# Kernel tuning notes

Measured on AMD Instinct MI355X. Metric: run time of the kernel, lower is better.

Reference implementation:

```python
import jax, jax.numpy as jnp
import numpy as np

# Problem constants (from init_kwargs)
NUM_NODES = 120000
NUM_MOVABLE = 100000
NUM_NETS = 100000
NUM_PINS = 400000
NBX = 256
NBY = 256
XL, XH, YL, YH = 0.0, 1000.0, 0.0, 1000.0
BSX = (XH - XL) / NBX  # bin_size_x
BSY = (YH - YL) / NBY  # bin_size_y
UNIT_H_CAP = 1.5  # unit_horizontal_routing_capacity
UNIT_V_CAP = 1.5  # unit_vertical_routing_capacity
MAX_RATE = 2.0    # max_route_opt_adjust_rate
MIN_RATE = 1.0 / MAX_RATE
EPS = 1e-6


def setup_inputs() -> dict:
    key = jax.random.key(0)
    k1, k2, k3, k4, k5, k6, k7, k8 = jax.random.split(key, 8)
    pos = jnp.concatenate([
        jax.random.uniform(k1, (NUM_NODES,), jnp.float32, XL, XH - 10.0),
        jax.random.uniform(k2, (NUM_NODES,), jnp.float32, YL, YH - 10.0)])
    pin_pos = jnp.concatenate([
        jax.random.uniform(k3, (NUM_PINS,), jnp.float32, XL, XH),
        jax.random.uniform(k4, (NUM_PINS,), jnp.float32, YL, YH)])
    node_size_x = jax.random.uniform(k5, (NUM_NODES,), jnp.float32, 1.0, 8.0)
    node_size_y = jax.random.uniform(k6, (NUM_NODES,), jnp.float32, 1.0, 4.0)
    flat_netpin = jax.random.randint(k7, (NUM_PINS,), 0, NUM_PINS, jnp.int32)
    inner = jnp.sort(jax.random.randint(k8, (NUM_NETS - 1,), 0, NUM_PINS, jnp.int32))
    netpin_start = jnp.concatenate([
        jnp.zeros((1,), jnp.int32), inner, jnp.full((1,), NUM_PINS, jnp.int32)])
    return dict(pos=pos, pin_pos=pin_pos, node_size_x=node_size_x,
                node_size_y=node_size_y, netpin_start=netpin_start,
                flat_netpin=flat_netpin)


def _bin_overlap(lo, hi, origin, bin_size, nbins):
    # lo, hi: [K] interval per item; returns [K, nbins] overlap length with each bin
    edges = origin + jnp.arange(nbins, dtype=lo.dtype) * bin_size  # [nbins]
    return jnp.clip(jnp.minimum(hi[:, None], edges + bin_size)
                    - jnp.maximum(lo[:, None], edges), 0.0)


def reference(pos, pin_pos, node_size_x, node_size_y, netpin_start, flat_netpin):
    num_pins = flat_netpin.shape[0]
    # --- per-net bounding boxes from ragged netpin lists (CSR) ---
    slot = jnp.arange(num_pins, dtype=jnp.int32)
    net_id = jnp.clip(jnp.searchsorted(netpin_start, slot, side='right') - 1,
                      0, NUM_NETS - 1)
    px = pin_pos[flat_netpin]
    py = pin_pos[num_pins + flat_netpin]
    xmin = jax.ops.segment_min(px, net_id, NUM_NETS, indices_are_sorted=True)
    xmax = jax.ops.segment_max(px, net_id, NUM_NETS, indices_are_sorted=True)
    ymin = jax.ops.segment_min(py, net_id, NUM_NETS, indices_are_sorted=True)
    ymax = jax.ops.segment_max(py, net_id, NUM_NETS, indices_are_sorted=True)
    valid = (xmax >= xmin) & (ymax >= ymin)  # nets with >=1 pin
    span_x = jnp.where(valid, xmax - xmin, 0.0)
    span_y = jnp.where(valid, ymax - ymin, 0.0)
    # RUDY demand density: horizontal demand per unit area = 1/span_y, etc.
    coef_h = jnp.where(valid & (span_y > EPS), 1.0 / jnp.maximum(span_y, EPS), 0.0)
    coef_v = jnp.where(valid & (span_x > EPS), 1.0 / jnp.maximum(span_x, EPS), 0.0)
    xmin_c = jnp.where(valid, xmin, XL)
    xmax_c = jnp.where(valid, xmax, XL)
    ymin_c = jnp.where(valid, ymin, YL)
    ymax_c = jnp.where(valid, ymax, YL)
    # separable bin overlaps: [N, NBX], [N, NBY]
    ox = _bin_overlap(xmin_c, xmax_c, XL, BSX, NBX)
    oy = _bin_overlap(ymin_c, ymax_c, YL, BSY, NBY)
    # scatter demand into 2D bin grid (rank-1 per net, summed via einsum)
    H = jnp.einsum('nx,ny->xy', ox * coef_h[:, None], oy)
    V = jnp.einsum('nx,ny->xy', ox * coef_v[:, None], oy)
    # capacity adjustment + clamp
    bin_area = BSX * BSY
    util = jnp.maximum(H / (bin_area * UNIT_H_CAP), V / (bin_area * UNIT_V_CAP))
    util = jnp.clip(util, MIN_RATE, MAX_RATE)
    # --- gather bin utilization back per movable node ---
    nxl = pos[:NUM_MOVABLE]
    nyl = pos[NUM_NODES:NUM_NODES + NUM_MOVABLE]
    nxh = nxl + node_size_x[:NUM_MOVABLE]
    nyh = nyl + node_size_y[:NUM_MOVABLE]
    nox = _bin_overlap(nxl, nxh, XL, BSX, NBX)  # [M, NBX]
    noy = _bin_overlap(nyl, nyh, YL, BSY, NBY)  # [M, NBY]
    instance_route_area = jnp.einsum('mx,xy,my->m', nox, util, noy)
    return instance_route_area
```

## Files before the change

### kernel.cpp

```cpp
#include <hip/hip_runtime.h>

#define NUM_NODES   120000
#define NUM_MOVABLE 100000
#define NUM_NETS    100000
#define NUM_PINS    400000
#define NBX 256
#define NBY 256
#define GRID (NBX*NBY)

constexpr float BSX      = 1000.0f / 256.0f;
constexpr float INV_BS   = 256.0f / 1000.0f;
constexpr float BIN_AREA = BSX * BSX;
constexpr float EPSV     = 1e-6f;


__global__ void init_bbox(float4* __restrict__ bbox) {
    int n = blockIdx.x * 256 + threadIdx.x;
    if (n < NUM_NETS) {
        float inf = __uint_as_float(0x7F800000u);
        bbox[n] = make_float4(inf, inf, 0.0f, 0.0f);
    }
}

__global__ void pin_bbox(const float* __restrict__ pin_pos,
                         const int* __restrict__ netpin_start,
                         const int* __restrict__ flat_netpin,
                         float4* __restrict__ bbox) {
    int t = blockIdx.x * 256 + threadIdx.x;
    int key = -4;
    int net = -1, segend = -1;
    float xmn = 3.4e38f, xmx = -3.4e38f, ymn = 3.4e38f, ymx = -3.4e38f;
    if (t < NUM_PINS) {
        int lo = 0, hi = NUM_NETS + 1;
        while (lo < hi) {
            int mid = (lo + hi) >> 1;
            if (netpin_start[mid] <= t) lo = mid + 1; else hi = mid;
        }
        net = min(lo - 1, NUM_NETS - 1);
        int s = netpin_start[net];
        segend = netpin_start[net + 1];
        key = (net << 1) | (s == t ? 1 : 0);
        int p = flat_netpin[t];
        float px = pin_pos[p];
        float py = pin_pos[NUM_PINS + p];
        xmn = px; xmx = px; ymn = py; ymx = py;
    }
    int lane = threadIdx.x & 63;
    for (int d = 1; d < 64; d <<= 1) {
        int   ku = __shfl_up(key, d);
        float a  = __shfl_up(xmn, d);
        float b  = __shfl_up(xmx, d);
        float c  = __shfl_up(ymn, d);
        float e  = __shfl_up(ymx, d);
        if (lane >= d && (ku >> 1) == (key >> 1)) {
            xmn = fminf(xmn, a); xmx = fmaxf(xmx, b);
            ymn = fminf(ymn, c); ymx = fmaxf(ymx, e);
            key |= (ku & 1);
        }
    }
    int nextkey = __shfl_down(key, 1);
    if (t >= NUM_PINS || net < 0) return;
    bool netchg = (lane == 63) ? false : ((nextkey >> 1) != (key >> 1));
    bool tail   = (lane == 63) || netchg;
    if (!tail) return;
    bool true_end  = netchg || (segend == t + 1);
    bool contained = (key & 1) != 0;
    if (contained && true_end) {
        bbox[net] = make_float4(xmn, ymn, xmx, ymx);
    } else {
        unsigned* b = (unsigned*)(bbox + net);
        atomicMin(b + 0, __float_as_uint(xmn));
        atomicMin(b + 1, __float_as_uint(ymn));
        atomicMax(b + 2, __float_as_uint(xmx));
        atomicMax(b + 3, __float_as_uint(ymx));
    }
}

__global__ __launch_bounds__(1024) void splat_rows(
        const float4* __restrict__ bbox,
        float* __restrict__ A_h, float* __restrict__ B_h,
        float* __restrict__ A_v, float* __restrict__ B_v) {
    int bx = blockIdx.x;
    int t  = threadIdx.x;
    __shared__ float F[8][NBY];
    for (int i = t; i < 8 * NBY; i += 1024) ((float*)F)[i] = 0.0f;
    __syncthreads();

    for (int n = t; n < NUM_NETS; n += 1024) {
        float4 b = bbox[n];
        float span_x = b.z - b.x, span_y = b.w - b.y;
        float coef_h = (span_y > EPSV) ? 1.0f / span_y : 0.0f;
        float coef_v = (span_x > EPSV) ? 1.0f / span_x : 0.0f;
        if (coef_h == 0.0f && coef_v == 0.0f) continue;
        int bxl = min((int)(b.x * INV_BS), NBX - 1);
        int bxh = min((int)(b.z * INV_BS), NBX - 1);
        if (bxl != bx && bxh != bx) continue;
        int byl = min((int)(b.y * INV_BS), NBY - 1);
        int byh = min((int)(b.w * INV_BS), NBY - 1);
        float ryl = (float)(byl + 1) * BSX - b.y;
        float ryh = (float)(byh + 1) * BSX - b.w;
        #pragma unroll
        for (int side = 0; side < 2; ++side) {
            bool active = (side == 0) ? (bxl == bx) : (bxh == bx);
            if (!active) continue;
            float rx = (side == 0) ? ((float)(bxl + 1) * BSX - b.x)
                                   : ((float)(bxh + 1) * BSX - b.z);
            float s0 = (side == 0) ? 1.0f : -1.0f;
            if (coef_h != 0.0f) {
                float w0 = s0 * coef_h, w1 = -s0 * coef_h;
                atomicAdd(&F[0][byl], w0 * rx  * ryl);
                atomicAdd(&F[1][byl], w0 * rx  * BSX);
                atomicAdd(&F[2][byl], w0 * BSX * ryl);
                atomicAdd(&F[3][byl], w0 * BSX * BSX);
                atomicAdd(&F[0][byh], w1 * rx  * ryh);
                atomicAdd(&F[1][byh], w1 * rx  * BSX);
                atomicAdd(&F[2][byh], w1 * BSX * ryh);
                atomicAdd(&F[3][byh], w1 * BSX * BSX);
            }
            if (coef_v != 0.0f) {
                float w0 = s0 * coef_v, w1 = -s0 * coef_v;
                atomicAdd(&F[4][byl], w0 * rx  * ryl);
                atomicAdd(&F[5][byl], w0 * rx  * BSX);
                atomicAdd(&F[6][byl], w0 * BSX * ryl);
                atomicAdd(&F[7][byl], w0 * BSX * BSX);
                atomicAdd(&F[4][byh], w1 * rx  * ryh);
                atomicAdd(&F[5][byh], w1 * rx  * BSX);
                atomicAdd(&F[6][byh], w1 * BSX * ryh);
                atomicAdd(&F[7][byh], w1 * BSX * BSX);
            }
        }
    }
    __syncthreads();

    int g = t >> 8, y = t & 255;
    float* f = F[2 * g + 1];
    for (int d = 1; d < 256; d <<= 1) {
        float add = (y >= d) ? f[y - d] : 0.0f;
        __syncthreads();
        f[y] += add;
        __syncthreads();
    }
    float ex = (y > 0) ? F[2 * g + 1][y - 1] : 0.0f;
    float val = F[2 * g][y] + ex;
    float* outs[4] = {A_h, B_h, A_v, B_v};
    outs[g][bx * NBY + y] = val;
}

__global__ void scan_x_util(const float* __restrict__ A_h, const float* __restrict__ B_h,
                            const float* __restrict__ A_v, const float* __restrict__ B_v,
                            float* __restrict__ util) {
    int y = blockIdx.x, x = threadIdx.x;
    int idx = x * NBY + y;
    __shared__ float2 tmp[NBX];
    tmp[x] = make_float2(B_h[idx], B_v[idx]);
    __syncthreads();
    for (int d = 1; d < 256; d <<= 1) {
        float2 add = (x >= d) ? tmp[x - d] : make_float2(0.f, 0.f);
        __syncthreads();
        tmp[x].x += add.x; tmp[x].y += add.y;
        __syncthreads();
    }
    float2 ex = (x > 0) ? tmp[x - 1] : make_float2(0.f, 0.f);
    float H = A_h[idx] + ex.x;
    float V = A_v[idx] + ex.y;
    float u = fmaxf(H, V) * (1.0f / (BIN_AREA * 1.5f));
    util[idx] = fminf(fmaxf(u, 0.5f), 2.0f);
}

__global__ void node_area(const float* __restrict__ pos,
                          const float* __restrict__ nsx,
                          const float* __restrict__ nsy,
                          const float* __restrict__ util,
                          float* __restrict__ out) {
    int m = blockIdx.x * 256 + threadIdx.x;
    if (m >= NUM_MOVABLE) return;
    float xl = pos[m];
    float yl = pos[NUM_NODES + m];
    float xh = xl + nsx[m];
    float yh = yl + nsy[m];
    int bx0 = max(0, min((int)(xl * INV_BS), NBX - 1));
    int bx1 = max(0, min((int)(xh * INV_BS), NBX - 1));
    int by0 = max(0, min((int)(yl * INV_BS), NBY - 1));
    int by1 = max(0, min((int)(yh * INV_BS), NBY - 1));
    float acc = 0.0f;
    for (int bx = bx0; bx <= bx1; ++bx) {
        float ox = fminf(xh, (float)(bx + 1) * BSX) - fmaxf(xl, (float)bx * BSX);
        if (ox <= 0.0f) continue;
        const float* urow = util + bx * NBY;
        float inner = 0.0f;
        for (int by = by0; by <= by1; ++by) {
            float oy = fminf(yh, (float)(by + 1) * BSX) - fmaxf(yl, (float)by * BSX);
            if (oy > 0.0f) inner += oy * urow[by];
        }
        acc += ox * inner;
    }
    out[m] = acc;
}

extern "C" void kernel_launch(void* const* d_in, const int* in_sizes, int n_in,
                              void* d_out, int out_size, void* d_ws, size_t ws_size,
                              hipStream_t stream) {
    const float* pos          = (const float*)d_in[0];
    const float* pin_pos      = (const float*)d_in[1];
    const float* node_size_x  = (const float*)d_in[2];
    const float* node_size_y  = (const float*)d_in[3];
    const int*   netpin_start = (const int*)d_in[4];
    const int*   flat_netpin  = (const int*)d_in[5];

    float4* bbox = (float4*)d_ws;
    float*  A_h  = (float*)(bbox + NUM_NETS);
    float*  B_h  = A_h + GRID;
    float*  A_v  = B_h + GRID;
    float*  B_v  = A_v + GRID;
    float*  util = B_v + GRID;
    float*  out  = (float*)d_out;

    init_bbox<<<(NUM_NETS + 255) / 256, 256, 0, stream>>>(bbox);
    pin_bbox<<<(NUM_PINS + 255) / 256, 256, 0, stream>>>(
        pin_pos, netpin_start, flat_netpin, bbox);
    splat_rows<<<NBX, 1024, 0, stream>>>(bbox, A_h, B_h, A_v, B_v);
    scan_x_util<<<NBY, NBX, 0, stream>>>(A_h, B_h, A_v, B_v, util);
    node_area<<<(NUM_MOVABLE + 255) / 256, 256, 0, stream>>>(
        pos, node_size_x, node_size_y, util, out);
}
```

Measured before the change: 148.6 us.

## Bucket nets by x-column before splatting instead of scanning all nets per block

Adds a scatter kernel that appends each net's index, tagged with its side, into fixed-capacity per-x-column buckets using global atomic counters. Each splat_rows block then reads only the nets in its own column instead of every block scanning all 100k bounding boxes. The intermediate A/B grids are also stored transposed so the x-direction scan reads contiguous memory. The trade-off is an extra kernel, global atomics, and a fixed per-column capacity of 2048: entries past that are silently dropped, which gives wrong results for denser columns.

Result: slower. 168.6 us (+13.5%).

```diff
diff --git a/kernel.cpp b/kernel.cpp
--- a/kernel.cpp
+++ b/kernel.cpp
@@ -7,6 +7,7 @@
 #define NBX 256
 #define NBY 256
 #define GRID (NBX*NBY)
+#define CAP 2048
 
 constexpr float BSX      = 1000.0f / 256.0f;
 constexpr float INV_BS   = 256.0f / 1000.0f;
@@ -14,12 +15,13 @@
 constexpr float EPSV     = 1e-6f;
 
 
-__global__ void init_bbox(float4* __restrict__ bbox) {
-    int n = blockIdx.x * 256 + threadIdx.x;
-    if (n < NUM_NETS) {
+__global__ void init_ws(float4* __restrict__ bbox, unsigned* __restrict__ count) {
+    int t = blockIdx.x * 256 + threadIdx.x;
+    if (t < NUM_NETS) {
         float inf = __uint_as_float(0x7F800000u);
-        bbox[n] = make_float4(inf, inf, 0.0f, 0.0f);
-    }
+        bbox[t] = make_float4(inf, inf, 0.0f, 0.0f);
+    }
+    if (t < 256 * 16) count[t] = 0u;
 }
 
 __global__ void pin_bbox(const float* __restrict__ pin_pos,
@@ -76,58 +78,76 @@
     }
 }
 
+__global__ void scatter_nets(const float4* __restrict__ bbox,
+                             unsigned* __restrict__ count,
+                             unsigned* __restrict__ entries) {
+    int n = blockIdx.x * 256 + threadIdx.x;
+    if (n >= NUM_NETS) return;
+    float4 b = bbox[n];
+    float span_x = b.z - b.x, span_y = b.w - b.y;
+    bool h = span_y > EPSV, v = span_x > EPSV;
+    if (!h && !v) return;
+    int bxl = min((int)(b.x * INV_BS), NBX - 1);
+    int bxh = min((int)(b.z * INV_BS), NBX - 1);
+    unsigned p0 = atomicAdd(count + bxl * 16, 1u);
+    if (p0 < CAP) entries[bxl * CAP + p0] = (unsigned)(n << 1);
+    unsigned p1 = atomicAdd(count + bxh * 16, 1u);
+    if (p1 < CAP) entries[bxh * CAP + p1] = (unsigned)(n << 1) | 1u;
+}
+
 __global__ __launch_bounds__(1024) void splat_rows(
         const float4* __restrict__ bbox,
-        float* __restrict__ A_h, float* __restrict__ B_h,
-        float* __restrict__ A_v, float* __restrict__ B_v) {
+        const unsigned* __restrict__ count,
+        const unsigned* __restrict__ entries,
+        float* __restrict__ A_hT, float* __restrict__ B_hT,
+        float* __restrict__ A_vT, float* __restrict__ B_vT) {
     int bx = blockIdx.x;
     int t  = threadIdx.x;
     __shared__ float F[8][NBY];
     for (int i = t; i < 8 * NBY; i += 1024) ((float*)F)[i] = 0.0f;
     __syncthreads();
 
-    for (int n = t; n < NUM_NETS; n += 1024) {
+    int cnt = (int)min(count[bx * 16], (unsigned)CAP);
+    for (int i = t; i < cnt; i += 1024) {
+        unsigned e = entries[bx * CAP + i];
+        int n = (int)(e >> 1), side = (int)(e & 1u);
         float4 b = bbox[n];
         float span_x = b.z - b.x, span_y = b.w - b.y;
         float coef_h = (span_y > EPSV) ? 1.0f / span_y : 0.0f;
         float coef_v = (span_x > EPSV) ? 1.0f / span_x : 0.0f;
-        if (coef_h == 0.0f && coef_v == 0.0f) continue;
-        int bxl = min((int)(b.x * INV_BS), NBX - 1);
-        int bxh = min((int)(b.z * INV_BS), NBX - 1);
-        if (bxl != bx && bxh != bx) continue;
         int byl = min((int)(b.y * INV_BS), NBY - 1);
         int byh = min((int)(b.w * INV_BS), NBY - 1);
         float ryl = (float)(byl + 1) * BSX - b.y;
         float ryh = (float)(byh + 1) * BSX - b.w;
-        #pragma unroll
-        for (int side = 0; side < 2; ++side) {
-            bool active = (side == 0) ? (bxl == bx) : (bxh == bx);
-            if (!active) continue;
-            float rx = (side == 0) ? ((float)(bxl + 1) * BSX - b.x)
-                                   : ((float)(bxh + 1) * BSX - b.z);
-            float s0 = (side == 0) ? 1.0f : -1.0f;
-            if (coef_h != 0.0f) {
-                float w0 = s0 * coef_h, w1 = -s0 * coef_h;
-                atomicAdd(&F[0][byl], w0 * rx  * ryl);
-                atomicAdd(&F[1][byl], w0 * rx  * BSX);
-                atomicAdd(&F[2][byl], w0 * BSX * ryl);
-                atomicAdd(&F[3][byl], w0 * BSX * BSX);
-                atomicAdd(&F[0][byh], w1 * rx  * ryh);
-                atomicAdd(&F[1][byh], w1 * rx  * BSX);
-                atomicAdd(&F[2][byh], w1 * BSX * ryh);
-                atomicAdd(&F[3][byh], w1 * BSX * BSX);
-            }
-            if (coef_v != 0.0f) {
-                float w0 = s0 * coef_v, w1 = -s0 * coef_v;
-                atomicAdd(&F[4][byl], w0 * rx  * ryl);
-                atomicAdd(&F[5][byl], w0 * rx  * BSX);
-                atomicAdd(&F[6][byl], w0 * BSX * ryl);
-                atomicAdd(&F[7][byl], w0 * BSX * BSX);
-                atomicAdd(&F[4][byh], w1 * rx  * ryh);
-                atomicAdd(&F[5][byh], w1 * rx  * BSX);
-                atomicAdd(&F[6][byh], w1 * BSX * ryh);
-                atomicAdd(&F[7][byh], w1 * BSX * BSX);
-            }
+        float rx, s0;
+        if (side == 0) {
+            int bxl = min((int)(b.x * INV_BS), NBX - 1);
+            rx = (float)(bxl + 1) * BSX - b.x; s0 = 1.0f;
+        } else {
+            int bxh = min((int)(b.z * INV_BS), NBX - 1);
+            rx = (float)(bxh + 1) * BSX - b.z; s0 = -1.0f;
+        }
+        if (coef_h != 0.0f) {
+            float w0 = s0 * coef_h, w1 = -s0 * coef_h;
+            atomicAdd(&F[0][byl], w0 * rx  * ryl);
+            atomicAdd(&F[1][byl], w0 * rx  * BSX);
+            atomicAdd(&F[2][byl], w0 * BSX * ryl);
+            atomicAdd(&F[3][byl], w0 * BSX * BSX);
+            atomicAdd(&F[0][byh], w1 * rx  * ryh);
+            atomicAdd(&F[1][byh], w1 * rx  * BSX);
+            atomicAdd(&F[2][byh], w1 * BSX * ryh);
+            atomicAdd(&F[3][byh], w1 * BSX * BSX);
+        }
+        if (coef_v != 0.0f) {
+            float w0 = s0 * coef_v, w1 = -s0 * coef_v;
+            atomicAdd(&F[4][byl], w0 * rx  * ryl);
+            atomicAdd(&F[5][byl], w0 * rx  * BSX);
+            atomicAdd(&F[6][byl], w0 * BSX * ryl);
+            atomicAdd(&F[7][byl], w0 * BSX * BSX);
+            atomicAdd(&F[4][byh], w1 * rx  * ryh);
+            atomicAdd(&F[5][byh], w1 * rx  * BSX);
+            atomicAdd(&F[6][byh], w1 * BSX * ryh);
+            atomicAdd(&F[7][byh], w1 * BSX * BSX);
         }
     }
     __syncthreads();
@@ -140,19 +160,19 @@
         f[y] += add;
         __syncthreads();
     }
-    float ex = (y > 0) ? F[2 * g + 1][y - 1] : 0.0f;
+    float ex  = (y > 0) ? F[2 * g + 1][y - 1] : 0.0f;
     float val = F[2 * g][y] + ex;
-    float* outs[4] = {A_h, B_h, A_v, B_v};
-    outs[g][bx * NBY + y] = val;
-}
-
-__global__ void scan_x_util(const float* __restrict__ A_h, const float* __restrict__ B_h,
-                            const float* __restrict__ A_v, const float* __restrict__ B_v,
+    float* o  = (g == 0) ? A_hT : (g == 1) ? B_hT : (g == 2) ? A_vT : B_vT;
+    o[y * NBX + bx] = val;
+}
+
+__global__ void scan_x_util(const float* __restrict__ A_hT, const float* __restrict__ B_hT,
+                            const float* __restrict__ A_vT, const float* __restrict__ B_vT,
                             float* __restrict__ util) {
     int y = blockIdx.x, x = threadIdx.x;
-    int idx = x * NBY + y;
+    int idxT = y * NBX + x;
     __shared__ float2 tmp[NBX];
-    tmp[x] = make_float2(B_h[idx], B_v[idx]);
+    tmp[x] = make_float2(B_hT[idxT], B_vT[idxT]);
     __syncthreads();
     for (int d = 1; d < 256; d <<= 1) {
         float2 add = (x >= d) ? tmp[x - d] : make_float2(0.f, 0.f);
@@ -161,10 +181,10 @@
         __syncthreads();
     }
     float2 ex = (x > 0) ? tmp[x - 1] : make_float2(0.f, 0.f);
-    float H = A_h[idx] + ex.x;
-    float V = A_v[idx] + ex.y;
+    float H = A_hT[idxT] + ex.x;
+    float V = A_vT[idxT] + ex.y;
     float u = fmaxf(H, V) * (1.0f / (BIN_AREA * 1.5f));
-    util[idx] = fminf(fmaxf(u, 0.5f), 2.0f);
+    util[x * NBY + y] = fminf(fmaxf(u, 0.5f), 2.0f);
 }
 
 __global__ void node_area(const float* __restrict__ pos,
@@ -207,19 +227,22 @@
     const int*   netpin_start = (const int*)d_in[4];
     const int*   flat_netpin  = (const int*)d_in[5];
 
-    float4* bbox = (float4*)d_ws;
-    float*  A_h  = (float*)(bbox + NUM_NETS);
-    float*  B_h  = A_h + GRID;
-    float*  A_v  = B_h + GRID;
-    float*  B_v  = A_v + GRID;
-    float*  util = B_v + GRID;
-    float*  out  = (float*)d_out;
-
-    init_bbox<<<(NUM_NETS + 255) / 256, 256, 0, stream>>>(bbox);
+    float4*   bbox    = (float4*)d_ws;
+    unsigned* count   = (unsigned*)(bbox + NUM_NETS);
+    unsigned* entries = count + 256 * 16;
+    float*    A_hT    = (float*)(entries + 256 * CAP);
+    float*    B_hT    = A_hT + GRID;
+    float*    A_vT    = B_hT + GRID;
+    float*    B_vT    = A_vT + GRID;
+    float*    util    = B_vT + GRID;
+    float*    out     = (float*)d_out;
+
+    init_ws<<<(NUM_NETS + 255) / 256, 256, 0, stream>>>(bbox, count);
     pin_bbox<<<(NUM_PINS + 255) / 256, 256, 0, stream>>>(
         pin_pos, netpin_start, flat_netpin, bbox);
-    splat_rows<<<NBX, 1024, 0, stream>>>(bbox, A_h, B_h, A_v, B_v);
-    scan_x_util<<<NBY, NBX, 0, stream>>>(A_h, B_h, A_v, B_v, util);
+    scatter_nets<<<(NUM_NETS + 255) / 256, 256, 0, stream>>>(bbox, count, entries);
+    splat_rows<<<NBX, 1024, 0, stream>>>(bbox, count, entries, A_hT, B_hT, A_vT, B_vT);
+    scan_x_util<<<NBY, NBX, 0, stream>>>(A_hT, B_hT, A_vT, B_vT, util);
     node_area<<<(NUM_MOVABLE + 255) / 256, 256, 0, stream>>>(
         pos, node_size_x, node_size_y, util, out);
 }
```
